# Performance work log

Hardware: AMD Instinct MI355X
Metric: run time of the kernel (lower is better)

Reference implementation:

```python
import jax, jax.numpy as jnp
import numpy as np

B, N, L, C, H = 4, 4096, 1024, 1024, 16
D = C // H  # head_dim = 64
SCALE = 1.0 / np.sqrt(D)


def setup_inputs() -> dict:
    key = jax.random.key(0)
    ks = jax.random.split(key, 5)
    return {
        "x": jax.random.normal(ks[0], (B, N, C), dtype=jnp.float32),
        "query": jax.random.normal(ks[1], (B, L, C), dtype=jnp.float32),
        "Wq": jax.random.normal(ks[2], (C, C), dtype=jnp.float32) * 0.02,
        "Wkv": jax.random.normal(ks[3], (2 * C, C), dtype=jnp.float32) * 0.02,
        "Wproj": jax.random.normal(ks[4], (C, C), dtype=jnp.float32) * 0.02,
        "bproj": jnp.zeros((C,), dtype=jnp.float32),
    }


def reference(x, query, Wq, Wkv, Wproj, bproj):
    # q projection: [B,L,C] -> [B,H,L,D]
    q = (query @ Wq.T).reshape(B, L, H, D).transpose(0, 2, 1, 3)
    # kv projection: [B,N,2C] -> k,v each [B,H,N,D]
    kv = (x @ Wkv.T).reshape(B, N, 2, H, D).transpose(2, 0, 3, 1, 4)
    k, v = kv[0], kv[1]
    # unfused SDPA: explicit [B,H,L,N] score matrix (faithful to source)
    attn = jnp.einsum('bhld,bhnd->bhln', q, k) * SCALE
    attn = jax.nn.softmax(attn, axis=-1)
    out = jnp.einsum('bhln,bhnd->bhld', attn, v)  # [B,H,L,D]
    out = out.transpose(0, 2, 1, 3).reshape(B, L, C)
    return out @ Wproj.T + bproj
```

## Files before the change

### kernel.cpp

```cpp
#include <hip/hip_runtime.h>
#include <hip/hip_bf16.h>

typedef __attribute__((ext_vector_type(8))) short short8;
typedef __attribute__((ext_vector_type(4))) float floatx4;

#if __has_builtin(__builtin_amdgcn_exp2f)
#define EXP2(x) __builtin_amdgcn_exp2f(x)
#else
#define EXP2(x) exp2f(x)
#endif

#define BAR() __builtin_amdgcn_s_barrier()
#define FENCE() asm volatile("" ::: "memory")
#define WAIT_LGKM0() asm volatile("s_waitcnt lgkmcnt(0)" ::: "memory")
#define WAIT_VM(n) asm volatile("s_waitcnt vmcnt(" #n ")" ::: "memory")

__device__ __forceinline__ short f2bf(float f) {
  __hip_bfloat16 h = __float2bfloat16(f);
  return *reinterpret_cast<const short*>(&h);
}

__device__ __forceinline__ short8 cvt_f32x8_bf16(const float* __restrict__ p) {
  float4 a = *reinterpret_cast<const float4*>(p);
  float4 b = *reinterpret_cast<const float4*>(p + 4);
  short8 r;
  r[0] = f2bf(a.x); r[1] = f2bf(a.y); r[2] = f2bf(a.z); r[3] = f2bf(a.w);
  r[4] = f2bf(b.x); r[5] = f2bf(b.y); r[6] = f2bf(b.z); r[7] = f2bf(b.w);
  return r;
}

typedef const __attribute__((address_space(1))) void* gptr1;
typedef __attribute__((address_space(3))) void* lptr3;
__device__ __forceinline__ void gl_lds16(const void* g, void* l) {
  __builtin_amdgcn_global_load_lds((gptr1)g, (lptr3)l, 16, 0, 0);
}

__global__ __launch_bounds__(256)
void f32_to_bf16(const float* __restrict__ in, short* __restrict__ out, int n8) {
  int i = blockIdx.x * blockDim.x + threadIdx.x;
  if (i < n8) {
    short8 v = cvt_f32x8_bf16(in + (size_t)i * 8);
    *reinterpret_cast<short8*>(out + (size_t)i * 8) = v;
  }
}

__global__ __launch_bounds__(512, 2)
void gemm256_kv(const short* __restrict__ A, const short* __restrict__ B,
                short* __restrict__ k_out, short* __restrict__ vt,
                int M, int N, int K)
{
  __shared__ __align__(16) short lds[2][2][2][128 * 64];

  const int tid  = threadIdx.x;
  const int lane = tid & 63;
  const int w    = tid >> 6;
  const int wm   = w >> 2;
  const int wn   = w & 3;
  const int cl   = lane & 15;
  const int hi   = lane >> 4;
  const int srl  = lane >> 3;
  const int gch8 = (((lane & 7) ^ srl) << 3);

  const int ntile = N >> 8;
  int bid = blockIdx.x;
  { int cpx = gridDim.x >> 3; bid = (bid & 7) * cpx + (bid >> 3); }
  const int tm = bid / ntile, tn = bid % ntile;
  const int m0 = tm << 8, n0 = tn << 8;
  const int NT = K >> 6;

  auto stageA = [&](int par, int slot, int ktX) {
    #pragma unroll
    for (int j = 0; j < 2; ++j) {
      const int sr = (w << 4) + (j << 3) + srl;
      const int tr = ((sr >> 6) << 7) + (slot << 6) + (sr & 63);
      gl_lds16(A + (size_t)(m0 + tr) * K + ktX + gch8,
               (void*)&lds[par][0][slot][((w << 4) + (j << 3)) * 64]);
    }
  };
  auto stageB = [&](int par, int slot, int ktX) {
    #pragma unroll
    for (int j = 0; j < 2; ++j) {
      const int sr = (w << 4) + (j << 3) + srl;
      const int tr = ((sr >> 5) << 6) + (slot << 5) + (sr & 31);
      gl_lds16(B + (size_t)(n0 + tr) * K + ktX + gch8,
               (void*)&lds[par][1][slot][((w << 4) + (j << 3)) * 64]);
    }
  };

  const floatx4 fzero = {0.f, 0.f, 0.f, 0.f};
  floatx4 acc[8][4];
  #pragma unroll
  for (int m = 0; m < 8; ++m)
    #pragma unroll
    for (int n = 0; n < 4; ++n)
      acc[m][n] = fzero;

  short8 af[4][2], b0[2][2], b1[2][2];

  auto readA = [&](int par, int slot) {
    #pragma unroll
    for (int m = 0; m < 4; ++m)
      #pragma unroll
      for (int ks = 0; ks < 2; ++ks) {
        const int sr = (wm << 6) + (m << 4) + cl;
        const int cpos = ((((ks << 2) + hi) ^ (sr & 7)) << 3);
        af[m][ks] = *reinterpret_cast<const short8*>(&lds[par][0][slot][sr * 64 + cpos]);
      }
  };
  auto readB = [&](int par, int slot, short8 (&bf)[2][2]) {
    #pragma unroll
    for (int n = 0; n < 2; ++n)
      #pragma unroll
      for (int ks = 0; ks < 2; ++ks) {
        const int sr = (wn << 5) + (n << 4) + cl;
        const int cpos = ((((ks << 2) + hi) ^ (sr & 7)) << 3);
        bf[n][ks] = *reinterpret_cast<const short8*>(&lds[par][1][slot][sr * 64 + cpos]);
      }
  };

  #define QUAD(BF, MH, NH)                                                     \
    __builtin_amdgcn_s_setprio(1);                                             \
    _Pragma("unroll")                                                          \
    for (int ks = 0; ks < 2; ++ks)                                             \
      _Pragma("unroll")                                                        \
      for (int m = 0; m < 4; ++m)                                              \
        _Pragma("unroll")                                                      \
        for (int n = 0; n < 2; ++n)                                            \
          acc[(MH)*4 + m][(NH)*2 + n] = __builtin_amdgcn_mfma_f32_16x16x32_bf16( \
              af[m][ks], BF[n][ks], acc[(MH)*4 + m][(NH)*2 + n], 0, 0, 0);     \
    __builtin_amdgcn_s_setprio(0);

  stageA(0, 0, 0); stageB(0, 0, 0); stageB(0, 1, 0); stageA(0, 1, 0);
  stageA(1, 0, 64); stageB(1, 0, 64); stageB(1, 1, 64);
  WAIT_VM(6); BAR(); FENCE();

  for (int t = 0; t < NT; ++t) {
    const int p  = t & 1;
    const int pn = p ^ 1;
    int t1 = t + 1; if (t1 >= NT) t1 -= NT;
    int t2 = t + 2; if (t2 >= NT) t2 -= NT;
    const int kt1 = t1 << 6;
    const int kt2 = t2 << 6;

    readA(p, 0); readB(p, 0, b0);
    stageA(pn, 1, kt1);
    BAR(); WAIT_LGKM0();
    QUAD(b0, 0, 0);
    BAR(); FENCE();

    readB(p, 1, b1);
    stageA(p, 0, kt2);
    BAR(); WAIT_LGKM0();
    QUAD(b1, 0, 1);
    BAR(); FENCE();

    readA(p, 1);
    stageB(p, 0, kt2);
    BAR(); WAIT_LGKM0();
    QUAD(b0, 1, 0);
    BAR(); FENCE();

    stageB(p, 1, kt2);
    WAIT_VM(6);
    BAR(); WAIT_LGKM0();
    QUAD(b1, 1, 1);
    BAR(); FENCE();
  }
  WAIT_VM(0);

  const int rq = hi << 2;
  #pragma unroll
  for (int Mi = 0; Mi < 8; ++Mi) {
    #pragma unroll
    for (int Nn = 0; Nn < 4; ++Nn) {
      const int grow = m0 + wm * 128 + Mi * 16 + rq;
      const int gcol = n0 + wn * 64 + Nn * 16 + cl;
      if (gcol < 1024) {
        #pragma unroll
        for (int i = 0; i < 4; ++i)
          k_out[(size_t)(grow + i) * 1024 + gcol] = f2bf(acc[Mi][Nn][i]);
      } else {
        const int d  = gcol - 1024;
        const int bb = grow >> 12;
        const int nn = grow & 4095;
        size_t base = ((size_t)(bb * 16 + (d >> 6)) * 64 + (d & 63)) * 4096 + nn;
        short4 pk;
        pk.x = f2bf(acc[Mi][Nn][0]); pk.y = f2bf(acc[Mi][Nn][1]);
        pk.z = f2bf(acc[Mi][Nn][2]); pk.w = f2bf(acc[Mi][Nn][3]);
        *reinterpret_cast<short4*>(&vt[base]) = pk;
      }
    }
  }
}

template<int MODE>
__global__ __launch_bounds__(256, 2)
void gemm_bt(const short* __restrict__ A, const short* __restrict__ B,
             void* __restrict__ O0, const float* __restrict__ bias,
             int M, int N, int K, float oscale)
{
  __shared__ short As[128 * 64];
  __shared__ short Bs[128 * 64];

  const int tid  = threadIdx.x;
  const int lane = tid & 63;
  const int w    = tid >> 6;
  const int ntile = N >> 7;
  int bid = blockIdx.x;
  { int cpx = gridDim.x >> 3; bid = (bid & 7) * cpx + (bid >> 3); }
  const int tm = bid / ntile;
  const int tn = bid % ntile;
  const int m0 = tm << 7, n0 = tn << 7;
  const int wr = (w >> 1) << 6;
  const int wc = (w & 1) << 6;

  const int srow = lane >> 3;
  const int scol = (lane & 7) << 3;

  const floatx4 fzero = {0.f, 0.f, 0.f, 0.f};
  floatx4 acc[4][4];
  #pragma unroll
  for (int m = 0; m < 4; ++m)
    #pragma unroll
    for (int n = 0; n < 4; ++n)
      acc[m][n] = fzero;

  for (int kt = 0; kt < K; kt += 64) {
    #pragma unroll
    for (int i = 0; i < 4; ++i) {
      const int chunk = (w << 2) + i;
      const int row   = (chunk << 3) + srow;
      gl_lds16(A + (size_t)(m0 + row) * K + kt + scol, &As[chunk * 512]);
      gl_lds16(B + (size_t)(n0 + row) * K + kt + scol, &Bs[chunk * 512]);
    }
    __syncthreads();

    #pragma unroll
    for (int ks = 0; ks < 2; ++ks) {
      short8 af[4], bfr[4];
      #pragma unroll
      for (int m = 0; m < 4; ++m)
        af[m] = *reinterpret_cast<const short8*>(
            &As[(wr + m * 16 + (lane & 15)) * 64 + ks * 32 + ((lane >> 4) << 3)]);
      #pragma unroll
      for (int n = 0; n < 4; ++n)
        bfr[n] = *reinterpret_cast<const short8*>(
            &Bs[(wc + n * 16 + (lane & 15)) * 64 + ks * 32 + ((lane >> 4) << 3)]);
      #pragma unroll
      for (int m = 0; m < 4; ++m)
        #pragma unroll
        for (int n = 0; n < 4; ++n)
          acc[m][n] = __builtin_amdgcn_mfma_f32_16x16x32_bf16(af[m], bfr[n], acc[m][n], 0, 0, 0);
    }
    __syncthreads();
  }

  const int rq = (lane >> 4) << 2;
  const int cl = lane & 15;
  #pragma unroll
  for (int m = 0; m < 4; ++m) {
    #pragma unroll
    for (int n = 0; n < 4; ++n) {
      const int grow = m0 + wr + m * 16 + rq;
      const int gcol = n0 + wc + n * 16 + cl;
      if (MODE == 0) {
        short* o = (short*)O0;
        #pragma unroll
        for (int i = 0; i < 4; ++i)
          o[(size_t)(grow + i) * N + gcol] = f2bf(acc[m][n][i] * oscale);
      } else {
        float* o = (float*)O0;
        const float bv = bias[gcol];
        #pragma unroll
        for (int i = 0; i < 4; ++i)
          o[(size_t)(grow + i) * N + gcol] = acc[m][n][i] + bv;
      }
    }
  }
}

__global__ __launch_bounds__(256, 2)
void attn_fwd(const short* __restrict__ q_ws, const short* __restrict__ k_ws,
              const short* __restrict__ vt_ws, short* __restrict__ ao_ws)
{
  __shared__ __align__(16) short Ks[2][64 * 64];
  __shared__ __align__(16) short Vts[2][64 * 64];
  __shared__ __align__(16) short Pl[2][4][32 * 64];

  const int tid  = threadIdx.x;
  const int lane = tid & 63;
  const int w    = tid >> 6;
  const int i    = blockIdx.x;
  const int bh   = (i & 7) * 8 + (i >> 6);
  const int qt   = (i >> 3) & 7;
  const int b  = bh >> 4;
  const int h  = bh & 15;
  const int q0 = qt * 128 + w * 32;
  const int cl = lane & 15;
  const int hi = lane >> 4;
  const int rq = hi << 2;
  const int key7 = cl & 7;

  short8 qf[2][2];
  #pragma unroll
  for (int tt = 0; tt < 2; ++tt)
    #pragma unroll
    for (int ks = 0; ks < 2; ++ks) {
      size_t idx = (size_t)(b * 1024 + q0 + tt * 16 + cl) * 1024
                 + h * 64 + ks * 32 + (hi << 3);
      qf[tt][ks] = *reinterpret_cast<const short8*>(&q_ws[idx]);
    }

  int koff[2];
  #pragma unroll
  for (int ks = 0; ks < 2; ++ks)
    koff[ks] = cl * 64 + ((((ks << 2) + hi) ^ key7) << 3);
  const int pwc   = hi >> 1;
  const int pwoff = (hi & 1) << 2;
  int pwch[4];
  #pragma unroll
  for (int n = 0; n < 4; ++n)
    pwch[n] = ((((n << 1) + pwc) ^ key7) << 3) + pwoff + cl * 64;

  const floatx4 fzero = {0.f, 0.f, 0.f, 0.f};
  floatx4 o[2][4];
  floatx4 s[4][2];
  float lr[2][2] = {{0.f, 0.f}, {0.f, 0.f}};
  #pragma unroll
  for (int tt = 0; tt < 2; ++tt)
    #pragma unroll
    for (int nd = 0; nd < 4; ++nd) o[tt][nd] = fzero;

  const int c0    = w << 1;
  const int srow8 = lane >> 3;
  const int gch8  = (((lane & 7) ^ srow8) << 3);
  const short* kbase = k_ws + (size_t)(b * 4096 + (c0 << 3) + srow8) * 1024 + h * 64 + gch8;
  const short* vbase = vt_ws + ((size_t)bh * 64 + (c0 << 3) + srow8) * 4096 + gch8;

  auto stage = [&](int buf, int kv0) {
    gl_lds16(kbase + (size_t)kv0 * 1024,          (void*)&Ks[buf][c0 * 512]);
    gl_lds16(kbase + (size_t)kv0 * 1024 + 8192,   (void*)&Ks[buf][(c0 + 1) * 512]);
    gl_lds16(vbase + kv0,                          (void*)&Vts[buf][c0 * 512]);
    gl_lds16(vbase + kv0 + 8 * 4096,               (void*)&Vts[buf][(c0 + 1) * 512]);
  };

  auto zs = [&]() {
    #pragma unroll
    for (int n = 0; n < 4; ++n)
      #pragma unroll
      for (int tt = 0; tt < 2; ++tt) s[n][tt] = fzero;
  };
  auto qk = [&](const short* kb) {
    #pragma unroll
    for (int ks = 0; ks < 2; ++ks) {
      short8 kf[4];
      #pragma unroll
      for (int n = 0; n < 4; ++n)
        kf[n] = *reinterpret_cast<const short8*>(kb + koff[ks] + n * 1024);
      #pragma unroll
      for (int n = 0; n < 4; ++n)
        #pragma unroll
        for (int tt = 0; tt < 2; ++tt)
          s[n][tt] = __builtin_amdgcn_mfma_f32_16x16x32_bf16(kf[n], qf[tt][ks], s[n][tt], 0, 0, 0);
    }
  };
  auto pv = [&](const short* plb, const short* vb) {
    #pragma unroll
    for (int ks = 0; ks < 2; ++ks) {
      short8 pa[2], vf[4];
      #pragma unroll
      for (int tt = 0; tt < 2; ++tt)
        pa[tt] = *reinterpret_cast<const short8*>(plb + koff[ks] + tt * 1024);
      #pragma unroll
      for (int nd = 0; nd < 4; ++nd)
        vf[nd] = *reinterpret_cast<const short8*>(vb + koff[ks] + nd * 1024);
      #pragma unroll
      for (int tt = 0; tt < 2; ++tt)
        #pragma unroll
        for (int nd = 0; nd < 4; ++nd)
          o[tt][nd] = __builtin_amdgcn_mfma_f32_16x16x32_bf16(pa[tt], vf[nd], o[tt][nd], 0, 0, 0);
    }
  };
  auto smax = [&](short* plw) {
    #pragma unroll
    for (int tt = 0; tt < 2; ++tt)
      #pragma unroll
      for (int n = 0; n < 4; ++n) {
        short4 pk;
        #pragma unroll
        for (int ii = 0; ii < 4; ++ii) {
          float p = EXP2(s[n][tt][ii]);
          lr[tt][n & 1] += p;
          pk[ii] = f2bf(p);
        }
        *reinterpret_cast<short4*>(plw + tt * 1024 + pwch[n]) = pk;
      }
  };

  stage(0, 0);
  WAIT_VM(0); BAR(); FENCE();
  zs(); qk(&Ks[0][0]);
  stage(1, 64);
  smax(&Pl[0][w][0]);
  int pb = 0;

  for (int t = 0; t < 63; ++t) {
    const int cur = t & 1;
    WAIT_VM(0); BAR(); FENCE();
    __builtin_amdgcn_s_setprio(1);
    zs();
    qk(&Ks[cur ^ 1][0]);
    pv(&Pl[pb][w][0], &Vts[cur][0]);
    __builtin_amdgcn_s_setprio(0);
    FENCE(); BAR();
    stage(cur, ((t + 2) & 63) << 6);
    smax(&Pl[pb ^ 1][w][0]);
    pb ^= 1;
  }
  __builtin_amdgcn_s_setprio(1);
  pv(&Pl[pb][w][0], &Vts[1][0]);
  __builtin_amdgcn_s_setprio(0);
  WAIT_VM(0);

  float lf[2];
  #pragma unroll
  for (int tt = 0; tt < 2; ++tt) {
    float l = lr[tt][0] + lr[tt][1];
    l += __shfl_xor(l, 16);
    l += __shfl_xor(l, 32);
    lf[tt] = l;
  }
  #pragma unroll
  for (int m = 0; m < 2; ++m) {
    float inv[4];
    #pragma unroll
    for (int ii = 0; ii < 4; ++ii)
      inv[ii] = 1.f / __shfl(lf[m], rq + ii);
    #pragma unroll
    for (int nd = 0; nd < 4; ++nd)
      #pragma unroll
      for (int ii = 0; ii < 4; ++ii) {
        size_t idx = (size_t)(b * 1024 + q0 + m * 16 + rq + ii) * 1024
                   + h * 64 + nd * 16 + cl;
        ao_ws[idx] = f2bf(o[m][nd][ii] * inv[ii]);
      }
  }
}

extern "C" void kernel_launch(void* const* d_in, const int* in_sizes, int n_in,
                              void* d_out, int out_size, void* d_ws, size_t ws_size,
                              hipStream_t stream)
{
  const float* x     = (const float*)d_in[0];
  const float* query = (const float*)d_in[1];
  const float* Wq    = (const float*)d_in[2];
  const float* Wkv   = (const float*)d_in[3];
  const float* Wproj = (const float*)d_in[4];
  const float* bproj = (const float*)d_in[5];
  float* out = (float*)d_out;

  const float QSCALE = 0.18033688011112042f;

  char* ws = (char*)d_ws;
  short* k_ws   = (short*)(ws);
  short* vt_ws  = (short*)(ws + (32ull << 20));
  short* xb     = (short*)(ws + (64ull << 20));
  short* qb     = (short*)(ws + (64ull << 20));
  short* q_ws   = (short*)(ws + (72ull << 20));
  short* ao_ws  = (short*)(ws + (80ull << 20));
  short* wkvb   = (short*)(ws + (96ull << 20));
  short* wqb    = (short*)(ws + (100ull << 20));
  short* wprojb = (short*)(ws + (102ull << 20));

  f32_to_bf16<<<dim3(1024), 256, 0, stream>>>(Wkv,   wkvb,   (2048 * 1024) / 8);
  f32_to_bf16<<<dim3(512),  256, 0, stream>>>(Wq,    wqb,    (1024 * 1024) / 8);
  f32_to_bf16<<<dim3(512),  256, 0, stream>>>(Wproj, wprojb, (1024 * 1024) / 8);
  f32_to_bf16<<<dim3(8192), 256, 0, stream>>>(x,     xb,     (16384 * 1024) / 8);

  gemm256_kv<<<dim3(512), 512, 0, stream>>>(xb, wkvb, k_ws, vt_ws,
                                            16384, 2048, 1024);
  f32_to_bf16<<<dim3(2048), 256, 0, stream>>>(query, qb, (4096 * 1024) / 8);
  gemm_bt<0><<<dim3(256), 256, 0, stream>>>(qb, wqb, q_ws, nullptr,
                                            4096, 1024, 1024, QSCALE);
  attn_fwd<<<dim3(512), 256, 0, stream>>>(q_ws, k_ws, vt_ws, ao_ws);
  gemm_bt<2><<<dim3(256), 256, 0, stream>>>(ao_ws, wprojb, out, bproj,
                                            4096, 1024, 1024, 1.0f);
}
```

Measured before the change: 224.0 us.

## Split attention along KV into two halves with separate reduce kernel

The attention kernel now splits each (batch, head, query tile) over two KV halves, doubling the grid to 1024 blocks. Each half writes unnormalized bf16 partial outputs plus row sums, and a new reduce kernel adds the halves and normalizes. This is valid because the softmax uses no running max. The P tile in LDS drops from double to single buffer, with an added lgkm wait, so occupancy can rise to 3 blocks per CU. The three weight conversions are merged into one launch. In exchange it adds an extra pass over partial outputs, an extra launch, and an extra bf16 rounding of the partial results.

New measurement: 233.8 us. +4.4%, slower.

```diff
diff --git a/kernel.cpp b/kernel.cpp
--- a/kernel.cpp
+++ b/kernel.cpp
@@ -18,6 +18,10 @@
 __device__ __forceinline__ short f2bf(float f) {
   __hip_bfloat16 h = __float2bfloat16(f);
   return *reinterpret_cast<const short*>(&h);
+}
+__device__ __forceinline__ float bf2f(short s) {
+  unsigned u = ((unsigned)(unsigned short)s) << 16;
+  return __uint_as_float(u);
 }
 
 __device__ __forceinline__ short8 cvt_f32x8_bf16(const float* __restrict__ p) {
@@ -42,6 +46,19 @@
     short8 v = cvt_f32x8_bf16(in + (size_t)i * 8);
     *reinterpret_cast<short8*>(out + (size_t)i * 8) = v;
   }
+}
+
+__global__ __launch_bounds__(256)
+void conv_weights(const float* __restrict__ Wkv, const float* __restrict__ Wq,
+                  const float* __restrict__ Wproj, short* __restrict__ wkvb,
+                  short* __restrict__ wqb, short* __restrict__ wprojb) {
+  const float* src; short* dst; int off;
+  int i = blockIdx.x * 256 + threadIdx.x;
+  if (blockIdx.x < 1024)      { src = Wkv;   dst = wkvb;   off = i; }
+  else if (blockIdx.x < 1536) { src = Wq;    dst = wqb;    off = i - 1024 * 256; }
+  else                        { src = Wproj; dst = wprojb; off = i - 1536 * 256; }
+  short8 v = cvt_f32x8_bf16(src + (size_t)off * 8);
+  *reinterpret_cast<short8*>(dst + (size_t)off * 8) = v;
 }
 
 __global__ __launch_bounds__(512, 2)
@@ -279,20 +296,23 @@
   }
 }
 
-__global__ __launch_bounds__(256, 2)
+__global__ __launch_bounds__(256, 3)
 void attn_fwd(const short* __restrict__ q_ws, const short* __restrict__ k_ws,
-              const short* __restrict__ vt_ws, short* __restrict__ ao_ws)
+              const short* __restrict__ vt_ws, short* __restrict__ po,
+              float* __restrict__ pl)
 {
   __shared__ __align__(16) short Ks[2][64 * 64];
   __shared__ __align__(16) short Vts[2][64 * 64];
-  __shared__ __align__(16) short Pl[2][4][32 * 64];
+  __shared__ __align__(16) short Pl[4][32 * 64];
 
   const int tid  = threadIdx.x;
   const int lane = tid & 63;
   const int w    = tid >> 6;
   const int i    = blockIdx.x;
-  const int bh   = (i & 7) * 8 + (i >> 6);
+  const int bh   = (i & 7) * 8 + (i >> 7);
   const int qt   = (i >> 3) & 7;
+  const int kvh  = (i >> 6) & 1;
+  const int kvbase = kvh << 11;
   const int b  = bh >> 4;
   const int h  = bh & 15;
   const int q0 = qt * 128 + w * 32;
@@ -397,28 +417,27 @@
       }
   };
 
-  stage(0, 0);
+  stage(0, kvbase);
   WAIT_VM(0); BAR(); FENCE();
   zs(); qk(&Ks[0][0]);
-  stage(1, 64);
-  smax(&Pl[0][w][0]);
-  int pb = 0;
-
-  for (int t = 0; t < 63; ++t) {
+  stage(1, kvbase + 64);
+  smax(&Pl[w][0]);
+
+  for (int t = 0; t < 31; ++t) {
     const int cur = t & 1;
     WAIT_VM(0); BAR(); FENCE();
     __builtin_amdgcn_s_setprio(1);
     zs();
     qk(&Ks[cur ^ 1][0]);
-    pv(&Pl[pb][w][0], &Vts[cur][0]);
+    pv(&Pl[w][0], &Vts[cur][0]);
     __builtin_amdgcn_s_setprio(0);
     FENCE(); BAR();
-    stage(cur, ((t + 2) & 63) << 6);
-    smax(&Pl[pb ^ 1][w][0]);
-    pb ^= 1;
+    stage(cur, kvbase + (((t + 2) & 31) << 6));
+    WAIT_LGKM0();
+    smax(&Pl[w][0]);
   }
   __builtin_amdgcn_s_setprio(1);
-  pv(&Pl[pb][w][0], &Vts[1][0]);
+  pv(&Pl[w][0], &Vts[1][0]);
   __builtin_amdgcn_s_setprio(0);
   WAIT_VM(0);
 
@@ -430,21 +449,41 @@
     l += __shfl_xor(l, 32);
     lf[tt] = l;
   }
-  #pragma unroll
-  for (int m = 0; m < 2; ++m) {
-    float inv[4];
-    #pragma unroll
-    for (int ii = 0; ii < 4; ++ii)
-      inv[ii] = 1.f / __shfl(lf[m], rq + ii);
+  if (hi == 0) {
+    #pragma unroll
+    for (int tt = 0; tt < 2; ++tt)
+      pl[kvh * 65536 + bh * 1024 + q0 + tt * 16 + cl] = lf[tt];
+  }
+  #pragma unroll
+  for (int m = 0; m < 2; ++m)
     #pragma unroll
     for (int nd = 0; nd < 4; ++nd)
       #pragma unroll
       for (int ii = 0; ii < 4; ++ii) {
-        size_t idx = (size_t)(b * 1024 + q0 + m * 16 + rq + ii) * 1024
+        size_t idx = (size_t)kvh * 4194304
+                   + (size_t)(b * 1024 + q0 + m * 16 + rq + ii) * 1024
                    + h * 64 + nd * 16 + cl;
-        ao_ws[idx] = f2bf(o[m][nd][ii] * inv[ii]);
+        po[idx] = f2bf(o[m][nd][ii]);
       }
-  }
+}
+
+__global__ __launch_bounds__(256)
+void attn_reduce(const short* __restrict__ po, const float* __restrict__ pl,
+                 short* __restrict__ ao)
+{
+  int g = blockIdx.x * 256 + threadIdx.x;
+  int r  = g >> 7;
+  int c0 = (g & 127) << 3;
+  int b = r >> 10, qrow = r & 1023, h = c0 >> 6;
+  int li = (b * 16 + h) * 1024 + qrow;
+  float inv = 1.f / (pl[li] + pl[65536 + li]);
+  short8 v0 = *reinterpret_cast<const short8*>(&po[(size_t)r * 1024 + c0]);
+  short8 v1 = *reinterpret_cast<const short8*>(&po[4194304 + (size_t)r * 1024 + c0]);
+  short8 rv;
+  #pragma unroll
+  for (int j = 0; j < 8; ++j)
+    rv[j] = f2bf((bf2f(v0[j]) + bf2f(v1[j])) * inv);
+  *reinterpret_cast<short8*>(&ao[(size_t)r * 1024 + c0]) = rv;
 }
 
 extern "C" void kernel_launch(void* const* d_in, const int* in_sizes, int n_in,
@@ -466,23 +505,24 @@
   short* vt_ws  = (short*)(ws + (32ull << 20));
   short* xb     = (short*)(ws + (64ull << 20));
   short* qb     = (short*)(ws + (64ull << 20));
+  short* ao_ws  = (short*)(ws + (64ull << 20));
   short* q_ws   = (short*)(ws + (72ull << 20));
-  short* ao_ws  = (short*)(ws + (80ull << 20));
+  short* po     = (short*)(ws + (80ull << 20));
   short* wkvb   = (short*)(ws + (96ull << 20));
   short* wqb    = (short*)(ws + (100ull << 20));
+  float* pl     = (float*)(ws + (100ull << 20));
   short* wprojb = (short*)(ws + (102ull << 20));
 
-  f32_to_bf16<<<dim3(1024), 256, 0, stream>>>(Wkv,   wkvb,   (2048 * 1024) / 8);
-  f32_to_bf16<<<dim3(512),  256, 0, stream>>>(Wq,    wqb,    (1024 * 1024) / 8);
-  f32_to_bf16<<<dim3(512),  256, 0, stream>>>(Wproj, wprojb, (1024 * 1024) / 8);
-  f32_to_bf16<<<dim3(8192), 256, 0, stream>>>(x,     xb,     (16384 * 1024) / 8);
+  conv_weights<<<dim3(2048), 256, 0, stream>>>(Wkv, Wq, Wproj, wkvb, wqb, wprojb);
+  f32_to_bf16<<<dim3(8192), 256, 0, stream>>>(x, xb, (16384 * 1024) / 8);
 
   gemm256_kv<<<dim3(512), 512, 0, stream>>>(xb, wkvb, k_ws, vt_ws,
                                             16384, 2048, 1024);
   f32_to_bf16<<<dim3(2048), 256, 0, stream>>>(query, qb, (4096 * 1024) / 8);
   gemm_bt<0><<<dim3(256), 256, 0, stream>>>(qb, wqb, q_ws, nullptr,
                                             4096, 1024, 1024, QSCALE);
-  attn_fwd<<<dim3(512), 256, 0, stream>>>(q_ws, k_ws, vt_ws, ao_ws);
+  attn_fwd<<<dim3(1024), 256, 0, stream>>>(q_ws, k_ws, vt_ws, po, pl);
+  attn_reduce<<<dim3(2048), 256, 0, stream>>>(po, pl, ao_ws);
   gemm_bt<2><<<dim3(256), 256, 0, stream>>>(ao_ws, wprojb, out, bproj,
                                             4096, 1024, 1024, 1.0f);
 }
```

## Store V in MFMA fragment order and load it straight to registers

Applied to the files above, without the earlier changes.

The KV GEMM epilogue now writes V in a pre-swizzled per-lane fragment layout, so the attention kernel can load V operands directly from global memory into registers. This removes V staging through LDS and one barrier per iteration, and moves the K prefetch earlier in the loop. The three weight conversion launches are also merged into one kernel. The cost is higher register pressure from holding V fragments, plus exposed global-load latency on V if the prefetch does not cover it.

Result: no change. 220.5 us (-1.6%).

```diff
diff --git a/kernel.cpp b/kernel.cpp
--- a/kernel.cpp
+++ b/kernel.cpp
@@ -42,6 +42,19 @@
     short8 v = cvt_f32x8_bf16(in + (size_t)i * 8);
     *reinterpret_cast<short8*>(out + (size_t)i * 8) = v;
   }
+}
+
+__global__ __launch_bounds__(256)
+void conv_weights(const float* __restrict__ Wkv, const float* __restrict__ Wq,
+                  const float* __restrict__ Wproj, short* __restrict__ wkvb,
+                  short* __restrict__ wqb, short* __restrict__ wprojb) {
+  const float* src; short* dst; int off;
+  int i = blockIdx.x * 256 + threadIdx.x;
+  if (blockIdx.x < 1024)      { src = Wkv;   dst = wkvb;   off = i; }
+  else if (blockIdx.x < 1536) { src = Wq;    dst = wqb;    off = i - 1024 * 256; }
+  else                        { src = Wproj; dst = wprojb; off = i - 1536 * 256; }
+  short8 v = cvt_f32x8_bf16(src + (size_t)off * 8);
+  *reinterpret_cast<short8*>(dst + (size_t)off * 8) = v;
 }
 
 __global__ __launch_bounds__(512, 2)
@@ -180,10 +193,21 @@
         for (int i = 0; i < 4; ++i)
           k_out[(size_t)(grow + i) * 1024 + gcol] = f2bf(acc[Mi][Nn][i]);
       } else {
-        const int d  = gcol - 1024;
-        const int bb = grow >> 12;
-        const int nn = grow & 4095;
-        size_t base = ((size_t)(bb * 16 + (d >> 6)) * 64 + (d & 63)) * 4096 + nn;
+        const int dfull = gcol - 1024;
+        const int hh  = dfull >> 6;
+        const int d   = dfull & 63;
+        const int bb  = grow >> 12;
+        const int nn  = grow & 4095;
+        const int bh2 = bb * 16 + hh;
+        const int tt2 = nn >> 6;
+        const int kvi = nn & 63;
+        const int ksx = kvi >> 5;
+        const int hix = (kvi >> 3) & 3;
+        const int j0  = kvi & 7;
+        const int lnx = hix * 16 + (d & 15);
+        const int ndx = d >> 4;
+        size_t base = ((((size_t)bh2 * 64 + tt2) * 2 + ksx) * 4 + ndx) * 512
+                    + lnx * 8 + j0;
         short4 pk;
         pk.x = f2bf(acc[Mi][Nn][0]); pk.y = f2bf(acc[Mi][Nn][1]);
         pk.z = f2bf(acc[Mi][Nn][2]); pk.w = f2bf(acc[Mi][Nn][3]);
@@ -281,10 +305,9 @@
 
 __global__ __launch_bounds__(256, 2)
 void attn_fwd(const short* __restrict__ q_ws, const short* __restrict__ k_ws,
-              const short* __restrict__ vt_ws, short* __restrict__ ao_ws)
+              const short* __restrict__ vfrag, short* __restrict__ ao_ws)
 {
   __shared__ __align__(16) short Ks[2][64 * 64];
-  __shared__ __align__(16) short Vts[2][64 * 64];
   __shared__ __align__(16) short Pl[2][4][32 * 64];
 
   const int tid  = threadIdx.x;
@@ -325,6 +348,7 @@
   const floatx4 fzero = {0.f, 0.f, 0.f, 0.f};
   floatx4 o[2][4];
   floatx4 s[4][2];
+  short8 vf[2][4];
   float lr[2][2] = {{0.f, 0.f}, {0.f, 0.f}};
   #pragma unroll
   for (int tt = 0; tt < 2; ++tt)
@@ -335,13 +359,18 @@
   const int srow8 = lane >> 3;
   const int gch8  = (((lane & 7) ^ srow8) << 3);
   const short* kbase = k_ws + (size_t)(b * 4096 + (c0 << 3) + srow8) * 1024 + h * 64 + gch8;
-  const short* vbase = vt_ws + ((size_t)bh * 64 + (c0 << 3) + srow8) * 4096 + gch8;
-
-  auto stage = [&](int buf, int kv0) {
-    gl_lds16(kbase + (size_t)kv0 * 1024,          (void*)&Ks[buf][c0 * 512]);
-    gl_lds16(kbase + (size_t)kv0 * 1024 + 8192,   (void*)&Ks[buf][(c0 + 1) * 512]);
-    gl_lds16(vbase + kv0,                          (void*)&Vts[buf][c0 * 512]);
-    gl_lds16(vbase + kv0 + 8 * 4096,               (void*)&Vts[buf][(c0 + 1) * 512]);
+  auto stageK = [&](int buf, int kv0) {
+    gl_lds16(kbase + (size_t)kv0 * 1024,        (void*)&Ks[buf][c0 * 512]);
+    gl_lds16(kbase + (size_t)kv0 * 1024 + 8192, (void*)&Ks[buf][(c0 + 1) * 512]);
+  };
+  const short* vfb = vfrag + (size_t)bh * 262144 + lane * 8;
+  auto loadV = [&](int t) {
+    const short* p = vfb + (size_t)t * 4096;
+    #pragma unroll
+    for (int ks = 0; ks < 2; ++ks)
+      #pragma unroll
+      for (int nd = 0; nd < 4; ++nd)
+        vf[ks][nd] = *reinterpret_cast<const short8*>(p + (ks * 4 + nd) * 512);
   };
 
   auto zs = [&]() {
@@ -364,21 +393,18 @@
           s[n][tt] = __builtin_amdgcn_mfma_f32_16x16x32_bf16(kf[n], qf[tt][ks], s[n][tt], 0, 0, 0);
     }
   };
-  auto pv = [&](const short* plb, const short* vb) {
+  auto pv = [&](const short* plb) {
     #pragma unroll
     for (int ks = 0; ks < 2; ++ks) {
-      short8 pa[2], vf[4];
+      short8 pa[2];
       #pragma unroll
       for (int tt = 0; tt < 2; ++tt)
         pa[tt] = *reinterpret_cast<const short8*>(plb + koff[ks] + tt * 1024);
       #pragma unroll
-      for (int nd = 0; nd < 4; ++nd)
-        vf[nd] = *reinterpret_cast<const short8*>(vb + koff[ks] + nd * 1024);
-      #pragma unroll
       for (int tt = 0; tt < 2; ++tt)
         #pragma unroll
         for (int nd = 0; nd < 4; ++nd)
-          o[tt][nd] = __builtin_amdgcn_mfma_f32_16x16x32_bf16(pa[tt], vf[nd], o[tt][nd], 0, 0, 0);
+          o[tt][nd] = __builtin_amdgcn_mfma_f32_16x16x32_bf16(pa[tt], vf[ks][nd], o[tt][nd], 0, 0, 0);
     }
   };
   auto smax = [&](short* plw) {
@@ -397,28 +423,29 @@
       }
   };
 
-  stage(0, 0);
-  WAIT_VM(0); BAR(); FENCE();
+  stageK(0, 0);
+  stageK(1, 64);
+  loadV(0);
+  WAIT_VM(8); BAR(); FENCE();
   zs(); qk(&Ks[0][0]);
-  stage(1, 64);
   smax(&Pl[0][w][0]);
   int pb = 0;
 
   for (int t = 0; t < 63; ++t) {
     const int cur = t & 1;
-    WAIT_VM(0); BAR(); FENCE();
+    WAIT_VM(8); BAR(); FENCE();
+    stageK(cur, ((t + 2) & 63) << 6);
     __builtin_amdgcn_s_setprio(1);
     zs();
     qk(&Ks[cur ^ 1][0]);
-    pv(&Pl[pb][w][0], &Vts[cur][0]);
+    pv(&Pl[pb][w][0]);
     __builtin_amdgcn_s_setprio(0);
-    FENCE(); BAR();
-    stage(cur, ((t + 2) & 63) << 6);
+    loadV(t + 1);
     smax(&Pl[pb ^ 1][w][0]);
     pb ^= 1;
   }
   __builtin_amdgcn_s_setprio(1);
-  pv(&Pl[pb][w][0], &Vts[1][0]);
+  pv(&Pl[pb][w][0]);
   __builtin_amdgcn_s_setprio(0);
   WAIT_VM(0);
 
@@ -463,7 +490,7 @@
 
   char* ws = (char*)d_ws;
   short* k_ws   = (short*)(ws);
-  short* vt_ws  = (short*)(ws + (32ull << 20));
+  short* vfrag  = (short*)(ws + (32ull << 20));
   short* xb     = (short*)(ws + (64ull << 20));
   short* qb     = (short*)(ws + (64ull << 20));
   short* q_ws   = (short*)(ws + (72ull << 20));
@@ -472,17 +499,15 @@
   short* wqb    = (short*)(ws + (100ull << 20));
   short* wprojb = (short*)(ws + (102ull << 20));
 
-  f32_to_bf16<<<dim3(1024), 256, 0, stream>>>(Wkv,   wkvb,   (2048 * 1024) / 8);
-  f32_to_bf16<<<dim3(512),  256, 0, stream>>>(Wq,    wqb,    (1024 * 1024) / 8);
-  f32_to_bf16<<<dim3(512),  256, 0, stream>>>(Wproj, wprojb, (1024 * 1024) / 8);
-  f32_to_bf16<<<dim3(8192), 256, 0, stream>>>(x,     xb,     (16384 * 1024) / 8);
-
-  gemm256_kv<<<dim3(512), 512, 0, stream>>>(xb, wkvb, k_ws, vt_ws,
+  conv_weights<<<dim3(2048), 256, 0, stream>>>(Wkv, Wq, Wproj, wkvb, wqb, wprojb);
+  f32_to_bf16<<<dim3(8192), 256, 0, stream>>>(x, xb, (16384 * 1024) / 8);
+
+  gemm256_kv<<<dim3(512), 512, 0, stream>>>(xb, wkvb, k_ws, vfrag,
                                             16384, 2048, 1024);
   f32_to_bf16<<<dim3(2048), 256, 0, stream>>>(query, qb, (4096 * 1024) / 8);
   gemm_bt<0><<<dim3(256), 256, 0, stream>>>(qb, wqb, q_ws, nullptr,
                                             4096, 1024, 1024, QSCALE);
-  attn_fwd<<<dim3(512), 256, 0, stream>>>(q_ws, k_ws, vt_ws, ao_ws);
+  attn_fwd<<<dim3(512), 256, 0, stream>>>(q_ws, k_ws, vfrag, ao_ws);
   gemm_bt<2><<<dim3(256), 256, 0, stream>>>(ao_ws, wprojb, out, bproj,
                                             4096, 1024, 1024, 1.0f);
 }
```

## Triple-buffer attention K/V tiles, compute row sums via MFMA, merge weight casts

Applied to the files above, without the earlier changes.

The attention kernel now uses three LDS buffers for K and V tiles. Staging of the next tile is issued right after the barrier, which removes the second barrier per iteration. Softmax row sums are no longer accumulated with scalar adds and cross-lane shuffles; an extra MFMA against a ones vector folds them into the PV product, and QK accumulation starts from zero inside the MFMA chain. The three weight-conversion launches are merged into one kernel. The trade-offs are more LDS per block, which may limit occupancy, and row sums taken from bf16-rounded probabilities.

Result: no change. 225.3 us (+0.6%).

```diff
diff --git a/kernel.cpp b/kernel.cpp
--- a/kernel.cpp
+++ b/kernel.cpp
@@ -42,6 +42,19 @@
     short8 v = cvt_f32x8_bf16(in + (size_t)i * 8);
     *reinterpret_cast<short8*>(out + (size_t)i * 8) = v;
   }
+}
+
+__global__ __launch_bounds__(256)
+void conv_weights(const float* __restrict__ Wkv, const float* __restrict__ Wq,
+                  const float* __restrict__ Wproj, short* __restrict__ wkvb,
+                  short* __restrict__ wqb, short* __restrict__ wprojb) {
+  const float* src; short* dst; int off;
+  int i = blockIdx.x * 256 + threadIdx.x;
+  if (blockIdx.x < 1024)      { src = Wkv;   dst = wkvb;   off = i; }
+  else if (blockIdx.x < 1536) { src = Wq;    dst = wqb;    off = i - 1024 * 256; }
+  else                        { src = Wproj; dst = wprojb; off = i - 1536 * 256; }
+  short8 v = cvt_f32x8_bf16(src + (size_t)off * 8);
+  *reinterpret_cast<short8*>(dst + (size_t)off * 8) = v;
 }
 
 __global__ __launch_bounds__(512, 2)
@@ -283,8 +296,8 @@
 void attn_fwd(const short* __restrict__ q_ws, const short* __restrict__ k_ws,
               const short* __restrict__ vt_ws, short* __restrict__ ao_ws)
 {
-  __shared__ __align__(16) short Ks[2][64 * 64];
-  __shared__ __align__(16) short Vts[2][64 * 64];
+  __shared__ __align__(16) short Ks[3][64 * 64];
+  __shared__ __align__(16) short Vts[3][64 * 64];
   __shared__ __align__(16) short Pl[2][4][32 * 64];
 
   const int tid  = threadIdx.x;
@@ -324,12 +337,17 @@
 
   const floatx4 fzero = {0.f, 0.f, 0.f, 0.f};
   floatx4 o[2][4];
+  floatx4 ol[2];
   floatx4 s[4][2];
-  float lr[2][2] = {{0.f, 0.f}, {0.f, 0.f}};
-  #pragma unroll
-  for (int tt = 0; tt < 2; ++tt)
+  short8 vones;
+  #pragma unroll
+  for (int j = 0; j < 8; ++j) vones[j] = (short)0x3F80;
+  #pragma unroll
+  for (int tt = 0; tt < 2; ++tt) {
+    ol[tt] = fzero;
     #pragma unroll
     for (int nd = 0; nd < 4; ++nd) o[tt][nd] = fzero;
+  }
 
   const int c0    = w << 1;
   const int srow8 = lane >> 3;
@@ -344,25 +362,21 @@
     gl_lds16(vbase + kv0 + 8 * 4096,               (void*)&Vts[buf][(c0 + 1) * 512]);
   };
 
-  auto zs = [&]() {
+  auto qk = [&](const short* kb) {
+    short8 kf[2][4];
+    #pragma unroll
+    for (int ks = 0; ks < 2; ++ks)
+      #pragma unroll
+      for (int n = 0; n < 4; ++n)
+        kf[ks][n] = *reinterpret_cast<const short8*>(kb + koff[ks] + n * 1024);
     #pragma unroll
     for (int n = 0; n < 4; ++n)
       #pragma unroll
-      for (int tt = 0; tt < 2; ++tt) s[n][tt] = fzero;
-  };
-  auto qk = [&](const short* kb) {
-    #pragma unroll
-    for (int ks = 0; ks < 2; ++ks) {
-      short8 kf[4];
-      #pragma unroll
-      for (int n = 0; n < 4; ++n)
-        kf[n] = *reinterpret_cast<const short8*>(kb + koff[ks] + n * 1024);
-      #pragma unroll
-      for (int n = 0; n < 4; ++n)
-        #pragma unroll
-        for (int tt = 0; tt < 2; ++tt)
-          s[n][tt] = __builtin_amdgcn_mfma_f32_16x16x32_bf16(kf[n], qf[tt][ks], s[n][tt], 0, 0, 0);
-    }
+      for (int tt = 0; tt < 2; ++tt)
+        s[n][tt] = __builtin_amdgcn_mfma_f32_16x16x32_bf16(
+            kf[1][n], qf[tt][1],
+            __builtin_amdgcn_mfma_f32_16x16x32_bf16(kf[0][n], qf[tt][0], fzero, 0, 0, 0),
+            0, 0, 0);
   };
   auto pv = [&](const short* plb, const short* vb) {
     #pragma unroll
@@ -375,10 +389,12 @@
       for (int nd = 0; nd < 4; ++nd)
         vf[nd] = *reinterpret_cast<const short8*>(vb + koff[ks] + nd * 1024);
       #pragma unroll
-      for (int tt = 0; tt < 2; ++tt)
+      for (int tt = 0; tt < 2; ++tt) {
+        ol[tt] = __builtin_amdgcn_mfma_f32_16x16x32_bf16(pa[tt], vones, ol[tt], 0, 0, 0);
         #pragma unroll
         for (int nd = 0; nd < 4; ++nd)
           o[tt][nd] = __builtin_amdgcn_mfma_f32_16x16x32_bf16(pa[tt], vf[nd], o[tt][nd], 0, 0, 0);
+      }
     }
   };
   auto smax = [&](short* plw) {
@@ -388,54 +404,42 @@
       for (int n = 0; n < 4; ++n) {
         short4 pk;
         #pragma unroll
-        for (int ii = 0; ii < 4; ++ii) {
-          float p = EXP2(s[n][tt][ii]);
-          lr[tt][n & 1] += p;
-          pk[ii] = f2bf(p);
-        }
+        for (int ii = 0; ii < 4; ++ii)
+          pk[ii] = f2bf(EXP2(s[n][tt][ii]));
         *reinterpret_cast<short4*>(plw + tt * 1024 + pwch[n]) = pk;
       }
   };
 
   stage(0, 0);
-  WAIT_VM(0); BAR(); FENCE();
-  zs(); qk(&Ks[0][0]);
   stage(1, 64);
+  WAIT_VM(4); BAR(); FENCE();
+  qk(&Ks[0][0]);
   smax(&Pl[0][w][0]);
   int pb = 0;
+  int i0 = 0, i1 = 1, i2 = 2;
 
   for (int t = 0; t < 63; ++t) {
-    const int cur = t & 1;
     WAIT_VM(0); BAR(); FENCE();
+    stage(i2, ((t + 2) & 63) << 6);
     __builtin_amdgcn_s_setprio(1);
-    zs();
-    qk(&Ks[cur ^ 1][0]);
-    pv(&Pl[pb][w][0], &Vts[cur][0]);
+    qk(&Ks[i1][0]);
+    pv(&Pl[pb][w][0], &Vts[i0][0]);
     __builtin_amdgcn_s_setprio(0);
-    FENCE(); BAR();
-    stage(cur, ((t + 2) & 63) << 6);
     smax(&Pl[pb ^ 1][w][0]);
     pb ^= 1;
+    int tmp = i0; i0 = i1; i1 = i2; i2 = tmp;
   }
   __builtin_amdgcn_s_setprio(1);
-  pv(&Pl[pb][w][0], &Vts[1][0]);
+  pv(&Pl[pb][w][0], &Vts[i0][0]);
   __builtin_amdgcn_s_setprio(0);
   WAIT_VM(0);
 
-  float lf[2];
-  #pragma unroll
-  for (int tt = 0; tt < 2; ++tt) {
-    float l = lr[tt][0] + lr[tt][1];
-    l += __shfl_xor(l, 16);
-    l += __shfl_xor(l, 32);
-    lf[tt] = l;
-  }
   #pragma unroll
   for (int m = 0; m < 2; ++m) {
     float inv[4];
     #pragma unroll
     for (int ii = 0; ii < 4; ++ii)
-      inv[ii] = 1.f / __shfl(lf[m], rq + ii);
+      inv[ii] = 1.f / ol[m][ii];
     #pragma unroll
     for (int nd = 0; nd < 4; ++nd)
       #pragma unroll
@@ -472,10 +476,8 @@
   short* wqb    = (short*)(ws + (100ull << 20));
   short* wprojb = (short*)(ws + (102ull << 20));
 
-  f32_to_bf16<<<dim3(1024), 256, 0, stream>>>(Wkv,   wkvb,   (2048 * 1024) / 8);
-  f32_to_bf16<<<dim3(512),  256, 0, stream>>>(Wq,    wqb,    (1024 * 1024) / 8);
-  f32_to_bf16<<<dim3(512),  256, 0, stream>>>(Wproj, wprojb, (1024 * 1024) / 8);
-  f32_to_bf16<<<dim3(8192), 256, 0, stream>>>(x,     xb,     (16384 * 1024) / 8);
+  conv_weights<<<dim3(2048), 256, 0, stream>>>(Wkv, Wq, Wproj, wkvb, wqb, wprojb);
+  f32_to_bf16<<<dim3(8192), 256, 0, stream>>>(x, xb, (16384 * 1024) / 8);
 
   gemm256_kv<<<dim3(512), 512, 0, stream>>>(xb, wkvb, k_ws, vt_ws,
                                             16384, 2048, 1024);
```
